# Kernel tuning notes

Hardware: AMD Instinct MI355X
Metric: run time of the kernel (lower is better)

Reference implementation:

```python
import jax, jax.numpy as jnp
import numpy as np

B, T, HIDDEN, QLR = 1, 2560, 7168, 1536
N_HEADS, HEAD_DIM, ROPE_DIM, TOPK = 64, 128, 64, 2048
LN_EPS = 1e-6


def _rope(x, cos, sin):
    # non-interleaved (half-split) rotary: pairs are (x[i], x[i+d/2])
    d = x.shape[-1] // 2
    x1, x2 = x[..., :d], x[..., d:]
    return jnp.concatenate([x1 * cos - x2 * sin, x1 * sin + x2 * cos], axis=-1)


def setup_inputs() -> dict:
    key = jax.random.key(0)
    ks = jax.random.split(key, 6)
    x = jax.random.normal(ks[0], (B, T, HIDDEN), dtype=jnp.float32)
    qr = jax.random.normal(ks[1], (B, T, QLR), dtype=jnp.float32)
    # rope tables (theta = 10000)
    inv_freq = 1.0 / (10000.0 ** (jnp.arange(0, ROPE_DIM, 2, dtype=jnp.float32) / ROPE_DIM))
    angles = jnp.arange(T, dtype=jnp.float32)[:, None] * inv_freq[None, :]  # [T, 32]
    freqs_cos = jnp.cos(angles)
    freqs_sin = jnp.sin(angles)
    # causal additive mask
    i = jnp.arange(T)
    mask = jnp.where(i[None, :, None] >= i[None, None, :], 0.0, -1e9).astype(jnp.float32)  # [1,T,T]
    # params (torch Linear stored transposed so y = x @ W)
    s = 0.02
    wq_b = jax.random.normal(ks[2], (QLR, N_HEADS * HEAD_DIM), dtype=jnp.float32) * s
    wk_w = jax.random.normal(ks[3], (HIDDEN, HEAD_DIM), dtype=jnp.float32) * s
    k_gamma = jnp.ones((HEAD_DIM,), dtype=jnp.float32)
    k_beta = jnp.zeros((HEAD_DIM,), dtype=jnp.float32)
    wproj = jax.random.normal(ks[4], (HIDDEN, N_HEADS), dtype=jnp.float32) * s
    return {"x": x, "qr": qr, "freqs_cos": freqs_cos, "freqs_sin": freqs_sin,
            "mask": mask, "wq_b": wq_b, "wk_w": wk_w, "k_gamma": k_gamma,
            "k_beta": k_beta, "wproj": wproj}


def reference(x, qr, freqs_cos, freqs_sin, mask, wq_b, wk_w, k_gamma, k_beta, wproj):
    bsz, seqlen, _ = x.shape
    # queries
    q = (qr @ wq_b).reshape(bsz, seqlen, N_HEADS, HEAD_DIM)
    q_pe, q_nope = q[..., :ROPE_DIM], q[..., ROPE_DIM:]
    q_pe = _rope(q_pe, freqs_cos[None, :, None, :], freqs_sin[None, :, None, :])
    q = jnp.concatenate([q_pe, q_nope], axis=-1)  # [B,T,H,D]
    # keys: layernorm(wk(x))
    k = x @ wk_w  # [B,T,D]
    mu = jnp.mean(k, axis=-1, keepdims=True)
    var = jnp.mean(jnp.square(k - mu), axis=-1, keepdims=True)
    k = (k - mu) / jnp.sqrt(var + LN_EPS) * k_gamma + k_beta
    k_pe, k_nope = k[..., :ROPE_DIM], k[..., ROPE_DIM:]
    k_pe = _rope(k_pe, freqs_cos[None, :, :], freqs_sin[None, :, :])
    k = jnp.concatenate([k_pe, k_nope], axis=-1)  # [B,S,D]
    # per-head weights
    weights = (x @ wproj) * (N_HEADS ** -0.5) * (HEAD_DIM ** -0.5)  # [B,T,H]
    # relu score + weighted head reduce
    logits = jax.nn.relu(jnp.einsum('bthd,bsd->btsh', q, k))  # [B,T,S,H]
    index_score = jnp.einsum('btsh,bth->bts', logits, weights) + mask
    # top-k + scatter mask
    kk = min(TOPK, seqlen)
    _, topk_idx = jax.lax.top_k(index_score, kk)  # [B,T,K]
    index_mask = jnp.full((bsz, seqlen, seqlen), -1e9, dtype=jnp.float32)
    bi = jnp.arange(bsz)[:, None, None]
    ti = jnp.arange(seqlen)[None, :, None]
    index_mask = index_mask.at[bi, ti, topk_idx].set(0.0)
    return index_mask
```

## Files before the change

### kernel.cpp

```cpp
#include <hip/hip_runtime.h>
#include <cstdint>

#define T_SEQ   2560
#define HID     7168
#define QLRD    1536
#define NHEAD   64
#define HDIM    128
#define TOPK    2048
#define T0SEL   2048
#define NSEL    512

#define QHOFF 0
#define QLOFF 2097152
#define KOFF  4194304
#define WOFF  4521984
#define KHOFF 4554752
#define KLOFF 4718592
#define SOFF  5242880

typedef _Float16 half8 __attribute__((ext_vector_type(8)));
typedef _Float16 half4v __attribute__((ext_vector_type(4)));
typedef float    floatx16 __attribute__((ext_vector_type(16)));

__device__ __forceinline__ void lds_barrier() {
    asm volatile("s_waitcnt lgkmcnt(0)" ::: "memory");
    __builtin_amdgcn_s_barrier();
}

__global__ __launch_bounds__(384) void kw_kernel(
        const float* __restrict__ x, const float* __restrict__ wk,
        const float* __restrict__ wp, float* __restrict__ Pk,
        float* __restrict__ Pw, long pkstride, long pwstride, int klen) {
    const int t0 = blockIdx.x * 64;
    const int chunk = blockIdx.y;
    const int k0 = chunk * klen;
    const int kl = min(klen, HID - k0);
    const int steps = kl >> 5;
    float* pk = Pk + (size_t)chunk * pkstride;
    float* pw = Pw + (size_t)chunk * pwstride;

    const int tid = threadIdx.x;
    const int lane = tid & 63;
    const int wv = tid >> 6;
    const int wt = wv / 3;
    const int wn2 = wv % 3;
    const int l31 = lane & 31;
    const int kb = (lane >> 5) * 8;

    __shared__ __align__(16) _Float16 Ah[64 * 40];
    __shared__ __align__(16) _Float16 Al[64 * 40];
    __shared__ __align__(16) _Float16 Bh[192 * 40];
    __shared__ __align__(16) _Float16 Bl[192 * 40];

    const int am = tid >> 2;
    const int ak = (tid & 3) * 8;
    const int bkr = (tid / 48) * 4;
    const int bnr = (tid % 48) * 4;

    const float* aptr = x + (size_t)(t0 + am) * HID + k0 + ak;
    const float* bsrc; int bld, bcol;
    if (bnr < 128) { bsrc = wk; bld = 128; bcol = bnr; }
    else           { bsrc = wp; bld = 64;  bcol = bnr - 128; }
    const float* bptr = bsrc + (size_t)(k0 + bkr) * bld + bcol;

    float4 pa0, pa1;
    if (tid < 256) { pa0 = *(const float4*)(aptr + 0); pa1 = *(const float4*)(aptr + 4); }
    float4 pb0 = *(const float4*)(bptr + 0 * (size_t)bld);
    float4 pb1 = *(const float4*)(bptr + 1 * (size_t)bld);
    float4 pb2 = *(const float4*)(bptr + 2 * (size_t)bld);
    float4 pb3 = *(const float4*)(bptr + 3 * (size_t)bld);

    floatx16 Z = {0.f,0.f,0.f,0.f,0.f,0.f,0.f,0.f,0.f,0.f,0.f,0.f,0.f,0.f,0.f,0.f};
    floatx16 Chh0 = Z, Chl0 = Z, Clh0 = Z;
    floatx16 Chh1 = Z, Chl1 = Z, Clh1 = Z;

    for (int ks = 0; ks < steps; ++ks) {
        lds_barrier();
        if (tid < 256) {
            float av[8];
            *(float4*)&av[0] = pa0; *(float4*)&av[4] = pa1;
            half8 ha, la;
#pragma unroll
            for (int i = 0; i < 8; ++i) {
                float v = av[i];
                _Float16 hi = (_Float16)v;
                ha[i] = hi;
                la[i] = (_Float16)(v - (float)hi);
            }
            *(half8*)&Ah[am * 40 + ak] = ha;
            *(half8*)&Al[am * 40 + ak] = la;
        }
        {
            float bv[4][4];
            *(float4*)&bv[0][0] = pb0; *(float4*)&bv[1][0] = pb1;
            *(float4*)&bv[2][0] = pb2; *(float4*)&bv[3][0] = pb3;
#pragma unroll
            for (int j = 0; j < 4; ++j) {
                half4v hb, lb;
#pragma unroll
                for (int i = 0; i < 4; ++i) {
                    float v = bv[i][j] * 64.0f;
                    _Float16 hi = (_Float16)v;
                    hb[i] = hi;
                    lb[i] = (_Float16)(v - (float)hi);
                }
                *(half4v*)&Bh[(bnr + j) * 40 + bkr] = hb;
                *(half4v*)&Bl[(bnr + j) * 40 + bkr] = lb;
            }
        }
        lds_barrier();
        if (ks + 1 < steps) {
            aptr += 32; bptr += (size_t)32 * bld;
            if (tid < 256) { pa0 = *(const float4*)(aptr + 0); pa1 = *(const float4*)(aptr + 4); }
            pb0 = *(const float4*)(bptr + 0 * (size_t)bld);
            pb1 = *(const float4*)(bptr + 1 * (size_t)bld);
            pb2 = *(const float4*)(bptr + 2 * (size_t)bld);
            pb3 = *(const float4*)(bptr + 3 * (size_t)bld);
        }
        __builtin_amdgcn_sched_barrier(0);
#pragma unroll
        for (int c = 0; c < 2; ++c) {
            const int ka = c * 16 + kb;
            half8 ah  = *(const half8*)&Ah[(wt * 32 + l31) * 40 + ka];
            half8 al  = *(const half8*)&Al[(wt * 32 + l31) * 40 + ka];
            half8 bh0 = *(const half8*)&Bh[(wn2 * 64 + l31) * 40 + ka];
            half8 bl0 = *(const half8*)&Bl[(wn2 * 64 + l31) * 40 + ka];
            half8 bh1 = *(const half8*)&Bh[(wn2 * 64 + 32 + l31) * 40 + ka];
            half8 bl1 = *(const half8*)&Bl[(wn2 * 64 + 32 + l31) * 40 + ka];
            Chh0 = __builtin_amdgcn_mfma_f32_32x32x16_f16(ah, bh0, Chh0, 0, 0, 0);
            Chl0 = __builtin_amdgcn_mfma_f32_32x32x16_f16(ah, bl0, Chl0, 0, 0, 0);
            Clh0 = __builtin_amdgcn_mfma_f32_32x32x16_f16(al, bh0, Clh0, 0, 0, 0);
            Chh1 = __builtin_amdgcn_mfma_f32_32x32x16_f16(ah, bh1, Chh1, 0, 0, 0);
            Chl1 = __builtin_amdgcn_mfma_f32_32x32x16_f16(ah, bl1, Chl1, 0, 0, 0);
            Clh1 = __builtin_amdgcn_mfma_f32_32x32x16_f16(al, bh1, Clh1, 0, 0, 0);
        }
    }

    const int rbase = wt * 32 + 4 * (lane >> 5);
#pragma unroll
    for (int r = 0; r < 16; ++r) {
        int trow = t0 + rbase + (r & 3) + 8 * (r >> 2);
        float v0 = ((Chh0[r] + Chl0[r]) + Clh0[r]) * 0.015625f;
        float v1 = ((Chh1[r] + Chl1[r]) + Clh1[r]) * 0.015625f;
        int c0 = wn2 * 64 + l31;
        if (wn2 < 2) {
            pk[(size_t)trow * 128 + c0] = v0;
            pk[(size_t)trow * 128 + c0 + 32] = v1;
        } else if (trow >= T0SEL) {
            pw[(size_t)(trow - T0SEL) * 64 + c0 - 128] = v0;
            pw[(size_t)(trow - T0SEL) * 64 + c0 - 96] = v1;
        }
    }
}

__global__ void reduce2_kernel(float* __restrict__ dk, const float* __restrict__ sk,
                               long kstr, float* __restrict__ dw,
                               const float* __restrict__ sw, long wstr, int nchunk) {
    int i = blockIdx.x * 256 + threadIdx.x;
    if (i < 327680) {
        float s = sk[i];
        for (int c = 1; c < nchunk; ++c) s += sk[(size_t)c * kstr + i];
        dk[i] = s;
    } else {
        int j = i - 327680;
        float s = sw[j];
        for (int c = 1; c < nchunk; ++c) s += sw[(size_t)c * wstr + j];
        dw[j] = s;
    }
}

__global__ void lnrope_kernel(const float* __restrict__ fcos, const float* __restrict__ fsin,
                              const float* __restrict__ gamma, const float* __restrict__ beta,
                              const float* __restrict__ Kbuf, float* __restrict__ Wbuf,
                              _Float16* __restrict__ KhG, _Float16* __restrict__ KlG) {
#pragma clang fp contract(off)
    const int s = blockIdx.x;
    const int d = threadIdx.x;
    __shared__ float red[128];
    __shared__ float kn[128];
    float kv = Kbuf[(size_t)s * 128 + d];
    red[d] = kv;
    __syncthreads();
    for (int off = 64; off > 0; off >>= 1) {
        if (d < off) red[d] += red[d + off];
        __syncthreads();
    }
    float mu = red[0] / 128.0f;
    __syncthreads();
    float dv = kv - mu;
    red[d] = dv * dv;
    __syncthreads();
    for (int off = 64; off > 0; off >>= 1) {
        if (d < off) red[d] += red[d + off];
        __syncthreads();
    }
    float var = red[0] / 128.0f;
    float nrm = dv / sqrtf(var + 1e-6f);
    nrm = nrm * gamma[d] + beta[d];
    kn[d] = nrm;
    __syncthreads();
    float o;
    if (d < 64) {
        int p = d & 31;
        float c = fcos[s * 32 + p], sn = fsin[s * 32 + p];
        if (d < 32) o = kn[d] * c - kn[d + 32] * sn;
        else        o = kn[d - 32] * sn + kn[d] * c;
    } else {
        o = kn[d];
    }
    _Float16 hi = (_Float16)o;
    _Float16 lo = (_Float16)(o - (float)hi);
    KhG[(size_t)s * 128 + d] = hi;
    KlG[(size_t)s * 128 + d] = lo;
    if (s >= T0SEL && d < 64) {
        Wbuf[(size_t)(s - T0SEL) * 64 + d] *= (0.125f * 0.08838834764831845f);
    }
}

__global__ __launch_bounds__(256, 2) void q_kernel(
        const float* __restrict__ qr, const float* __restrict__ wqb,
        const float* __restrict__ fcos, const float* __restrict__ fsin,
        _Float16* __restrict__ QhG, _Float16* __restrict__ QlG) {
    const int head = blockIdx.x;
    const int bx = blockIdx.y;
    const int tid = threadIdx.x;
    const int lane = tid & 63;
    const int wv = tid >> 6;
    const int wt = wv >> 1, wn = wv & 1;
    const int l31 = lane & 31;
    const int kb = (lane >> 5) * 8;

    __shared__ __align__(16) _Float16 Ah[64 * 40];
    __shared__ __align__(16) _Float16 Al[64 * 40];
    __shared__ __align__(16) _Float16 Bh[128 * 40];
    __shared__ __align__(16) _Float16 Bl[128 * 40];

    const int am = tid >> 2;
    const int ak = (tid & 3) * 8;
    const int bn = (tid & 31) * 4;
    const int bk = (tid >> 5) * 4;

    const float* aB = qr + (size_t)(T0SEL + bx * 64 + am) * QLRD + ak;
    const float* bB = wqb + (size_t)bk * 8192 + head * 128 + bn;

    float4 paA0, paA1, pbA0, pbA1, pbA2, pbA3;
    float4 paB0, paB1, pbB0, pbB1, pbB2, pbB3;

#define QLOADSET(PA0,PA1,PB0,PB1,PB2,PB3,KK) do {                              \
    const float* ap_ = aB + (size_t)(KK) * 32;                                 \
    const float* bp_ = bB + (size_t)(KK) * 32 * 8192;                          \
    PA0 = *(const float4*)(ap_ + 0);                                           \
    PA1 = *(const float4*)(ap_ + 4);                                           \
    PB0 = *(const float4*)(bp_ + 0 * 8192);                                    \
    PB1 = *(const float4*)(bp_ + 1 * 8192);                                    \
    PB2 = *(const float4*)(bp_ + 2 * 8192);                                    \
    PB3 = *(const float4*)(bp_ + 3 * 8192);                                    \
} while (0)

#define QCONVERT(PA0,PA1,PB0,PB1,PB2,PB3) do {                                 \
    float av[8];                                                               \
    *(float4*)&av[0] = PA0; *(float4*)&av[4] = PA1;                            \
    half8 ha, la;                                                              \
    _Pragma("unroll")                                                          \
    for (int i = 0; i < 8; ++i) {                                              \
        float v = av[i];                                                       \
        _Float16 hi = (_Float16)v;                                             \
        ha[i] = hi;                                                            \
        la[i] = (_Float16)(v - (float)hi);                                     \
    }                                                                          \
    *(half8*)&Ah[am * 40 + ak] = ha;                                           \
    *(half8*)&Al[am * 40 + ak] = la;                                           \
    float bv[4][4];                                                            \
    *(float4*)&bv[0][0] = PB0; *(float4*)&bv[1][0] = PB1;                      \
    *(float4*)&bv[2][0] = PB2; *(float4*)&bv[3][0] = PB3;                      \
    _Pragma("unroll")                                                          \
    for (int j = 0; j < 4; ++j) {                                              \
        half4v hb, lb;                                                         \
        _Pragma("unroll")                                                      \
        for (int i = 0; i < 4; ++i) {                                          \
            float v = bv[i][j] * 64.0f;                                        \
            _Float16 hi = (_Float16)v;                                         \
            hb[i] = hi;                                                        \
            lb[i] = (_Float16)(v - (float)hi);                                 \
        }                                                                      \
        *(half4v*)&Bh[(bn + j) * 40 + bk] = hb;                                \
        *(half4v*)&Bl[(bn + j) * 40 + bk] = lb;                                \
    }                                                                          \
} while (0)

#define QMFMA() do {                                                           \
    __builtin_amdgcn_s_setprio(1);                                             \
    _Pragma("unroll")                                                          \
    for (int c = 0; c < 2; ++c) {                                              \
        const int ka = c * 16 + kb;                                            \
        half8 ah = *(const half8*)&Ah[(wt * 32 + l31) * 40 + ka];              \
        half8 al = *(const half8*)&Al[(wt * 32 + l31) * 40 + ka];              \
        half8 bh0 = *(const half8*)&Bh[(wn * 64 + l31) * 40 + ka];             \
        half8 bl0 = *(const half8*)&Bl[(wn * 64 + l31) * 40 + ka];             \
        half8 bh1 = *(const half8*)&Bh[(wn * 64 + 32 + l31) * 40 + ka];        \
        half8 bl1 = *(const half8*)&Bl[(wn * 64 + 32 + l31) * 40 + ka];        \
        Chh0 = __builtin_amdgcn_mfma_f32_32x32x16_f16(ah, bh0, Chh0, 0, 0, 0); \
        Chl0 = __builtin_amdgcn_mfma_f32_32x32x16_f16(ah, bl0, Chl0, 0, 0, 0); \
        Clh0 = __builtin_amdgcn_mfma_f32_32x32x16_f16(al, bh0, Clh0, 0, 0, 0); \
        Chh1 = __builtin_amdgcn_mfma_f32_32x32x16_f16(ah, bh1, Chh1, 0, 0, 0); \
        Chl1 = __builtin_amdgcn_mfma_f32_32x32x16_f16(ah, bl1, Chl1, 0, 0, 0); \
        Clh1 = __builtin_amdgcn_mfma_f32_32x32x16_f16(al, bh1, Clh1, 0, 0, 0); \
    }                                                                          \
    __builtin_amdgcn_s_setprio(0);                                             \
} while (0)

    floatx16 Z = {0.f,0.f,0.f,0.f,0.f,0.f,0.f,0.f,0.f,0.f,0.f,0.f,0.f,0.f,0.f,0.f};
    floatx16 Chh0 = Z, Chl0 = Z, Clh0 = Z;
    floatx16 Chh1 = Z, Chl1 = Z, Clh1 = Z;

    const int steps = QLRD / 32;
    QLOADSET(paA0, paA1, pbA0, pbA1, pbA2, pbA3, 0);
    QLOADSET(paB0, paB1, pbB0, pbB1, pbB2, pbB3, 1);

    for (int ks = 0; ks < steps; ks += 2) {
        lds_barrier();
        QCONVERT(paA0, paA1, pbA0, pbA1, pbA2, pbA3);
        lds_barrier();
        QLOADSET(paA0, paA1, pbA0, pbA1, pbA2, pbA3, min(ks + 2, steps - 1));
        __builtin_amdgcn_sched_barrier(0);
        QMFMA();

        lds_barrier();
        QCONVERT(paB0, paB1, pbB0, pbB1, pbB2, pbB3);
        lds_barrier();
        QLOADSET(paB0, paB1, pbB0, pbB1, pbB2, pbB3, min(ks + 3, steps - 1));
        __builtin_amdgcn_sched_barrier(0);
        QMFMA();
    }
#undef QLOADSET
#undef QCONVERT
#undef QMFMA

    {
#pragma clang fp contract(off)
        const int tbase = bx * 64 + wt * 32 + 4 * (lane >> 5);
#pragma unroll
        for (int r = 0; r < 16; ++r) {
            int tl = tbase + (r & 3) + 8 * (r >> 2);
            float v0 = ((Chh0[r] + Chl0[r]) + Clh0[r]) * 0.015625f;
            float v1 = ((Chh1[r] + Chl1[r]) + Clh1[r]) * 0.015625f;
            float o0, o1;
            if (wn == 0) {
                int tg = T0SEL + tl;
                float c = fcos[tg * 32 + l31];
                float s = fsin[tg * 32 + l31];
                o0 = v0 * c - v1 * s;
                o1 = v0 * s + v1 * c;
            } else {
                o0 = v0; o1 = v1;
            }
            int d0 = wn * 64 + l31;
            size_t off = (size_t)head * 65536 + (size_t)tl * 128;
            _Float16 h0 = (_Float16)o0;
            _Float16 h1 = (_Float16)o1;
            QhG[off + d0] = h0;
            QlG[off + d0] = (_Float16)(o0 - (float)h0);
            QhG[off + d0 + 32] = h1;
            QlG[off + d0 + 32] = (_Float16)(o1 - (float)h1);
        }
    }
}

__global__ __launch_bounds__(256) void score_kernel(
        const _Float16* __restrict__ Qh, const _Float16* __restrict__ Ql,
        const _Float16* __restrict__ Kh, const _Float16* __restrict__ Kl,
        const float* __restrict__ Wbuf, float* __restrict__ S0,
        float* __restrict__ S1, int hcnt) {
    const int bid = blockIdx.x;
    const int tt0 = (bid & 15) * 32;
    const int s0  = (bid >> 4) * 128;
    const int hb  = blockIdx.y * hcnt;
    float* __restrict__ dst = blockIdx.y ? S1 : S0;
    const int tid = threadIdx.x;
    const int wv  = tid >> 6;
    const int lane = tid & 63;
    const int l31 = lane & 31;
    const int kb  = (lane >> 5) * 8;

    __shared__ __align__(16) _Float16 AhA[32 * 136];
    __shared__ __align__(16) _Float16 AlA[32 * 136];
    __shared__ __align__(16) _Float16 AhB[32 * 136];
    __shared__ __align__(16) _Float16 AlB[32 * 136];
    __shared__ float WsT[64 * 36];

    half8 Bh[8], Bl[8];
    {
        const int srow = s0 + wv * 32 + l31;
        const _Float16* kh = Kh + (size_t)srow * 128 + kb;
        const _Float16* kl = Kl + (size_t)srow * 128 + kb;
#pragma unroll
        for (int c = 0; c < 8; ++c) {
            Bh[c] = *(const half8*)(kh + c * 16);
            Bl[c] = *(const half8*)(kl + c * 16);
        }
    }
#pragma unroll
    for (int r = 0; r < 8; ++r) {
        int idx = tid + 256 * r;
        int row = idx >> 6, h = idx & 63;
        WsT[h * 36 + row] = Wbuf[(size_t)(tt0 + row) * 64 + h];
    }

    const int srow0 = tid >> 4;
    const int scc0  = (tid & 15) * 8;
    const int srow1 = srow0 + 16;
    const int scc1  = scc0;

    const _Float16* qhp = Qh + (size_t)hb * 65536 + (size_t)tt0 * 128;
    const _Float16* qlp = Ql + (size_t)hb * 65536 + (size_t)tt0 * 128;

    half8 sh0 = *(const half8*)&qhp[srow0 * 128 + scc0];
    half8 sh1 = *(const half8*)&qhp[srow1 * 128 + scc1];
    half8 sl0 = *(const half8*)&qlp[srow0 * 128 + scc0];
    half8 sl1 = *(const half8*)&qlp[srow1 * 128 + scc1];
    *(half8*)&AhA[srow0 * 136 + scc0] = sh0;
    *(half8*)&AhA[srow1 * 136 + scc1] = sh1;
    *(half8*)&AlA[srow0 * 136 + scc0] = sl0;
    *(half8*)&AlA[srow1 * 136 + scc1] = sl1;
    qhp += 65536; qlp += 65536;
    sh0 = *(const half8*)&qhp[srow0 * 128 + scc0];
    sh1 = *(const half8*)&qhp[srow1 * 128 + scc1];
    sl0 = *(const half8*)&qlp[srow0 * 128 + scc0];
    sl1 = *(const half8*)&qlp[srow1 * 128 + scc1];
    __builtin_amdgcn_sched_barrier(0);
    lds_barrier();

    float S[16];
#pragma unroll
    for (int r = 0; r < 16; ++r) S[r] = 0.0f;

#define SCORE_COMPUTE(AH, AL, HIDX)                                            \
    {                                                                          \
        floatx16 C0 = {0.f,0.f,0.f,0.f,0.f,0.f,0.f,0.f,                        \
                       0.f,0.f,0.f,0.f,0.f,0.f,0.f,0.f};                       \
        floatx16 C2 = C0, C3 = C0;                                             \
        __builtin_amdgcn_s_setprio(1);                                         \
        _Pragma("unroll")                                                      \
        for (int c = 0; c < 8; ++c) {                                          \
            half8 a_h = *(const half8*)&AH[l31 * 136 + c * 16 + kb];           \
            half8 a_l = *(const half8*)&AL[l31 * 136 + c * 16 + kb];           \
            C0 = __builtin_amdgcn_mfma_f32_32x32x16_f16(a_h, Bh[c], C0, 0, 0, 0); \
            C2 = __builtin_amdgcn_mfma_f32_32x32x16_f16(a_h, Bl[c], C2, 0, 0, 0); \
            C3 = __builtin_amdgcn_mfma_f32_32x32x16_f16(a_l, Bh[c], C3, 0, 0, 0); \
        }                                                                      \
        __builtin_amdgcn_s_setprio(0);                                         \
        const float* wb = &WsT[(HIDX) * 36 + 4 * (lane >> 5)];                 \
        float4 w0 = *(const float4*)(wb + 0);                                  \
        float4 w1 = *(const float4*)(wb + 8);                                  \
        float4 w2 = *(const float4*)(wb + 16);                                 \
        float4 w3 = *(const float4*)(wb + 24);                                 \
        float w[16] = {w0.x, w0.y, w0.z, w0.w, w1.x, w1.y, w1.z, w1.w,         \
                       w2.x, w2.y, w2.z, w2.w, w3.x, w3.y, w3.z, w3.w};        \
        _Pragma("unroll")                                                      \
        for (int r = 0; r < 16; ++r) {                                         \
            float L = (C0[r] + C2[r]) + C3[r];                                 \
            S[r] += w[r] * fmaxf(L, 0.0f);                                     \
        }                                                                      \
    }

    for (int h = 0; h < hcnt; h += 2) {
        SCORE_COMPUTE(AhA, AlA, hb + h)
        *(half8*)&AhB[srow0 * 136 + scc0] = sh0;
        *(half8*)&AhB[srow1 * 136 + scc1] = sh1;
        *(half8*)&AlB[srow0 * 136 + scc0] = sl0;
        *(half8*)&AlB[srow1 * 136 + scc1] = sl1;
        qhp += 65536; qlp += 65536;
        sh0 = *(const half8*)&qhp[srow0 * 128 + scc0];
        sh1 = *(const half8*)&qhp[srow1 * 128 + scc1];
        sl0 = *(const half8*)&qlp[srow0 * 128 + scc0];
        sl1 = *(const half8*)&qlp[srow1 * 128 + scc1];
        __builtin_amdgcn_sched_barrier(0);
        lds_barrier();

        SCORE_COMPUTE(AhB, AlB, hb + h + 1)
        *(half8*)&AhA[srow0 * 136 + scc0] = sh0;
        *(half8*)&AhA[srow1 * 136 + scc1] = sh1;
        *(half8*)&AlA[srow0 * 136 + scc0] = sl0;
        *(half8*)&AlA[srow1 * 136 + scc1] = sl1;
        qhp += 65536; qlp += 65536;
        sh0 = *(const half8*)&qhp[srow0 * 128 + scc0];
        sh1 = *(const half8*)&qhp[srow1 * 128 + scc1];
        sl0 = *(const half8*)&qlp[srow0 * 128 + scc0];
        sl1 = *(const half8*)&qlp[srow1 * 128 + scc1];
        __builtin_amdgcn_sched_barrier(0);
        lds_barrier();
    }
#undef SCORE_COMPUTE

    const int scol = s0 + wv * 32 + l31;
#pragma unroll
    for (int r = 0; r < 16; ++r) {
        int trow = tt0 + (r & 3) + 8 * (r >> 2) + 4 * (lane >> 5);
        dst[(size_t)trow * 2560 + scol] = S[r] + 0.0f;
    }
}

__global__ void finalize_kernel(float* __restrict__ out, const float* __restrict__ S1) {
    const int row_id = blockIdx.x;
    const int tid = threadIdx.x;

    if (row_id < T0SEL) {
        const float4 zero4 = make_float4(0.0f, 0.0f, 0.0f, 0.0f);
        const float4 neg4 = make_float4(-1000000000.0f, -1000000000.0f,
                                        -1000000000.0f, -1000000000.0f);
        for (int i = tid; i < T_SEQ / 4; i += 256) {
            *(float4*)&out[(size_t)row_id * T_SEQ + i * 4] = (i * 4 < TOPK) ? zero4 : neg4;
        }
        return;
    }

    const int t = row_id;
    const int n = t + 1;
    float* row = out + (size_t)t * T_SEQ;
    const float* s1p = S1 ? (S1 + (size_t)(t - T0SEL) * T_SEQ) : nullptr;

    __shared__ unsigned U[T_SEQ];
    __shared__ int hist[256];
    __shared__ int aux[256];
    __shared__ unsigned sh_prefix;
    __shared__ int sh_kneed;

    for (int i = tid; i < T_SEQ; i += 256) {
        unsigned u = 0u;
        if (i < n) {
            float sc = row[i];
            if (s1p) sc += s1p[i];
            int b = __float_as_int(sc);
            u = (b < 0) ? ~((unsigned)b) : (((unsigned)b) | 0x80000000u);
        }
        U[i] = u;
    }
    if (tid == 0) { sh_prefix = 0u; sh_kneed = TOPK; }
    __syncthreads();

    for (int pass = 0; pass < 4; ++pass) {
        const int shift = 24 - 8 * pass;
        const unsigned himask = (pass == 0) ? 0u : (0xFFFFFFFFu << (shift + 8));
        hist[tid] = 0;
        __syncthreads();
        const unsigned pre = sh_prefix;
        const int kneed = sh_kneed;
        for (int i = tid; i < T_SEQ; i += 256) {
            unsigned u = U[i];
            if ((u & himask) == pre) atomicAdd(&hist[(u >> shift) & 255], 1);
        }
        __syncthreads();
        aux[tid] = hist[tid];
        __syncthreads();
        for (int off = 1; off < 256; off <<= 1) {
            int a = (tid + off < 256) ? aux[tid + off] : 0;
            __syncthreads();
            aux[tid] += a;
            __syncthreads();
        }
        int above = (tid < 255) ? aux[tid + 1] : 0;
        if (above < kneed && kneed <= aux[tid]) {
            sh_prefix = pre | (((unsigned)tid) << shift);
            sh_kneed = kneed - above;
        }
        __syncthreads();
    }
    const unsigned theta = sh_prefix;
    const int r = sh_kneed;

    const int s_lo = tid * 10, s_hi = s_lo + 10;
    int c = 0;
    for (int s = s_lo; s < s_hi; ++s) c += (U[s] == theta);
    aux[tid] = c;
    __syncthreads();
    for (int off = 1; off < 256; off <<= 1) {
        int a = (tid >= off) ? aux[tid - off] : 0;
        __syncthreads();
        aux[tid] += a;
        __syncthreads();
    }
    int rank = aux[tid] - c;
    for (int s = s_lo; s < s_hi; ++s) {
        unsigned u = U[s];
        bool sel = (u > theta) || (u == theta && rank < r);
        if (u == theta) ++rank;
        row[s] = sel ? 0.0f : -1000000000.0f;
    }
}

extern "C" void kernel_launch(void* const* d_in, const int* in_sizes, int n_in,
                              void* d_out, int out_size, void* d_ws, size_t ws_size,
                              hipStream_t stream) {
    (void)in_sizes; (void)n_in; (void)out_size;
    const float* x     = (const float*)d_in[0];
    const float* qr    = (const float*)d_in[1];
    const float* fcos  = (const float*)d_in[2];
    const float* fsin  = (const float*)d_in[3];
    const float* wqb   = (const float*)d_in[5];
    const float* wk    = (const float*)d_in[6];
    const float* gamma = (const float*)d_in[7];
    const float* beta  = (const float*)d_in[8];
    const float* wp    = (const float*)d_in[9];

    float* out  = (float*)d_out;
    float* Kbuf = out + KOFF;
    float* Wbuf = out + WOFF;
    float* Sbuf = out + SOFF;
    _Float16* QhG = (_Float16*)(out + QHOFF);
    _Float16* QlG = (_Float16*)(out + QLOFF);
    _Float16* KhG = (_Float16*)(out + KHOFF);
    _Float16* KlG = (_Float16*)(out + KLOFF);

    const size_t need = (size_t)(6 * 327680 + 6 * 32768) * 4;
    int nchunk; int klen; float *Pk, *Pw; long pkstride, pwstride;
    if (ws_size >= need) {
        nchunk = 6; klen = 1216;
        Pk = (float*)d_ws;            pkstride = 327680;
        Pw = (float*)d_ws + 1966080;  pwstride = 32768;
    } else {
        nchunk = 2; klen = 3584;
        Pk = out + KOFF;  pkstride = 360448;
        Pw = out + WOFF;  pwstride = 360448;
    }

    const size_t s1_need = (size_t)NSEL * T_SEQ * sizeof(float);
    float* S1 = (ws_size >= s1_need) ? (float*)d_ws : nullptr;

    kw_kernel<<<dim3(40, nchunk), 384, 0, stream>>>(x, wk, wp, Pk, Pw, pkstride, pwstride, klen);
    reduce2_kernel<<<1408, 256, 0, stream>>>(Kbuf, Pk, pkstride, Wbuf, Pw, pwstride, nchunk);
    lnrope_kernel<<<T_SEQ, 128, 0, stream>>>(fcos, fsin, gamma, beta, Kbuf, Wbuf, KhG, KlG);
    q_kernel<<<dim3(64, 8), 256, 0, stream>>>(qr, wqb, fcos, fsin, QhG, QlG);
    if (S1) {
        score_kernel<<<dim3(320, 2), 256, 0, stream>>>(QhG, QlG, KhG, KlG, Wbuf, Sbuf, S1, 32);
    } else {
        score_kernel<<<dim3(320, 1), 256, 0, stream>>>(QhG, QlG, KhG, KlG, Wbuf, Sbuf, nullptr, 64);
    }
    finalize_kernel<<<T_SEQ, 256, 0, stream>>>(out, S1);
}
```

Baseline: 393.5 us.

## Double-buffer LDS tiles and XOR-swizzle layout in kw and q GEMM kernels

Both split-fp16 GEMM kernels (kw_kernel and q_kernel) get two LDS buffer sets. The MFMA work on one buffer now overlaps the fp32-to-fp16 conversion into the other, which cuts the two barriers per k-step down to one. An XOR swizzle on the k offset within each row is also applied to the LDS stores and reads to reduce bank conflicts. The cost is double the LDS footprint, which may lower occupancy, and q_kernel drops its second register prefetch set.

```diff
diff --git a/kernel.cpp b/kernel.cpp
--- a/kernel.cpp
+++ b/kernel.cpp
@@ -26,6 +26,8 @@
     asm volatile("s_waitcnt lgkmcnt(0)" ::: "memory");
     __builtin_amdgcn_s_barrier();
 }
+
+#define SWZ(row) ((((row) >> 3) & 3) << 3)
 
 __global__ __launch_bounds__(384) void kw_kernel(
         const float* __restrict__ x, const float* __restrict__ wk,
@@ -47,94 +49,125 @@
     const int l31 = lane & 31;
     const int kb = (lane >> 5) * 8;
 
-    __shared__ __align__(16) _Float16 Ah[64 * 40];
-    __shared__ __align__(16) _Float16 Al[64 * 40];
-    __shared__ __align__(16) _Float16 Bh[192 * 40];
-    __shared__ __align__(16) _Float16 Bl[192 * 40];
+    __shared__ __align__(16) _Float16 Ah0[64 * 40], Al0[64 * 40];
+    __shared__ __align__(16) _Float16 Bh0[192 * 40], Bl0[192 * 40];
+    __shared__ __align__(16) _Float16 Ah1[64 * 40], Al1[64 * 40];
+    __shared__ __align__(16) _Float16 Bh1[192 * 40], Bl1[192 * 40];
 
     const int am = tid >> 2;
     const int ak = (tid & 3) * 8;
+    const int akS = ak ^ SWZ(am);
     const int bkr = (tid / 48) * 4;
     const int bnr = (tid % 48) * 4;
 
-    const float* aptr = x + (size_t)(t0 + am) * HID + k0 + ak;
+    const float* aB = x + (size_t)(t0 + am) * HID + k0 + ak;
     const float* bsrc; int bld, bcol;
     if (bnr < 128) { bsrc = wk; bld = 128; bcol = bnr; }
     else           { bsrc = wp; bld = 64;  bcol = bnr - 128; }
-    const float* bptr = bsrc + (size_t)(k0 + bkr) * bld + bcol;
-
-    float4 pa0, pa1;
-    if (tid < 256) { pa0 = *(const float4*)(aptr + 0); pa1 = *(const float4*)(aptr + 4); }
-    float4 pb0 = *(const float4*)(bptr + 0 * (size_t)bld);
-    float4 pb1 = *(const float4*)(bptr + 1 * (size_t)bld);
-    float4 pb2 = *(const float4*)(bptr + 2 * (size_t)bld);
-    float4 pb3 = *(const float4*)(bptr + 3 * (size_t)bld);
+    const float* bB = bsrc + (size_t)(k0 + bkr) * bld + bcol;
+
+    float4 pa0, pa1, pb0, pb1, pb2, pb3;
+
+#define KWLOAD(KK) do {                                                        \
+    const float* ap_ = aB + (size_t)(KK) * 32;                                 \
+    const float* bp_ = bB + (size_t)(KK) * 32 * bld;                           \
+    if (tid < 256) { pa0 = *(const float4*)(ap_ + 0);                          \
+                     pa1 = *(const float4*)(ap_ + 4); }                        \
+    pb0 = *(const float4*)(bp_ + 0 * (size_t)bld);                             \
+    pb1 = *(const float4*)(bp_ + 1 * (size_t)bld);                             \
+    pb2 = *(const float4*)(bp_ + 2 * (size_t)bld);                             \
+    pb3 = *(const float4*)(bp_ + 3 * (size_t)bld);                             \
+} while (0)
+
+#define KWCONVERT(AH, AL, BH, BL) do {                                         \
+    if (tid < 256) {                                                           \
+        float av[8];                                                           \
+        *(float4*)&av[0] = pa0; *(float4*)&av[4] = pa1;                        \
+        half8 ha, la;                                                          \
+        _Pragma("unroll")                                                      \
+        for (int i = 0; i < 8; ++i) {                                          \
+            float v = av[i];                                                   \
+            _Float16 hi = (_Float16)v;                                         \
+            ha[i] = hi;                                                        \
+            la[i] = (_Float16)(v - (float)hi);                                 \
+        }                                                                      \
+        *(half8*)&AH[am * 40 + akS] = ha;                                      \
+        *(half8*)&AL[am * 40 + akS] = la;                                      \
+    }                                                                          \
+    {                                                                          \
+        float bv[4][4];                                                        \
+        *(float4*)&bv[0][0] = pb0; *(float4*)&bv[1][0] = pb1;                  \
+        *(float4*)&bv[2][0] = pb2; *(float4*)&bv[3][0] = pb3;                  \
+        _Pragma("unroll")                                                      \
+        for (int j = 0; j < 4; ++j) {                                          \
+            const int bkS = bkr ^ SWZ(bnr + j);                                \
+            half4v hb, lb;                                                     \
+            _Pragma("unroll")                                                  \
+            for (int i = 0; i < 4; ++i) {                                      \
+                float v = bv[i][j] * 64.0f;                                    \
+                _Float16 hi = (_Float16)v;                                     \
+                hb[i] = hi;                                                    \
+                lb[i] = (_Float16)(v - (float)hi);                             \
+            }                                                                  \
+            *(half4v*)&BH[(bnr + j) * 40 + bkS] = hb;                          \
+            *(half4v*)&BL[(bnr + j) * 40 + bkS] = lb;                          \
+        }                                                                      \
+    }                                                                          \
+} while (0)
+
+    const int rowA  = wt * 32 + l31;
+    const int xA    = SWZ(rowA);
+    const int rowB0 = wn2 * 64 + l31;
+    const int xB0   = SWZ(rowB0);
+    const int rowB1 = rowB0 + 32;
+    const int xB1   = SWZ(rowB1);
+
+#define KWMFMA(AH, AL, BH, BL) do {                                            \
+    __builtin_amdgcn_s_setprio(1);                                             \
+    _Pragma("unroll")                                                          \
+    for (int c = 0; c < 2; ++c) {                                              \
+        const int ka = c * 16 + kb;                                            \
+        half8 ah  = *(const half8*)&AH[rowA * 40 + (ka ^ xA)];                 \
+        half8 al  = *(const half8*)&AL[rowA * 40 + (ka ^ xA)];                 \
+        half8 bh0 = *(const half8*)&BH[rowB0 * 40 + (ka ^ xB0)];               \
+        half8 bl0 = *(const half8*)&BL[rowB0 * 40 + (ka ^ xB0)];               \
+        half8 bh1 = *(const half8*)&BH[rowB1 * 40 + (ka ^ xB1)];               \
+        half8 bl1 = *(const half8*)&BL[rowB1 * 40 + (ka ^ xB1)];               \
+        Chh0 = __builtin_amdgcn_mfma_f32_32x32x16_f16(ah, bh0, Chh0, 0, 0, 0); \
+        Chl0 = __builtin_amdgcn_mfma_f32_32x32x16_f16(ah, bl0, Chl0, 0, 0, 0); \
+        Clh0 = __builtin_amdgcn_mfma_f32_32x32x16_f16(al, bh0, Clh0, 0, 0, 0); \
+        Chh1 = __builtin_amdgcn_mfma_f32_32x32x16_f16(ah, bh1, Chh1, 0, 0, 0); \
+        Chl1 = __builtin_amdgcn_mfma_f32_32x32x16_f16(ah, bl1, Chl1, 0, 0, 0); \
+        Clh1 = __builtin_amdgcn_mfma_f32_32x32x16_f16(al, bh1, Clh1, 0, 0, 0); \
+    }                                                                          \
+    __builtin_amdgcn_s_setprio(0);                                             \
+} while (0)
 
     floatx16 Z = {0.f,0.f,0.f,0.f,0.f,0.f,0.f,0.f,0.f,0.f,0.f,0.f,0.f,0.f,0.f,0.f};
     floatx16 Chh0 = Z, Chl0 = Z, Clh0 = Z;
     floatx16 Chh1 = Z, Chl1 = Z, Clh1 = Z;
 
-    for (int ks = 0; ks < steps; ++ks) {
+    KWLOAD(0);
+    KWCONVERT(Ah0, Al0, Bh0, Bl0);
+    KWLOAD(1);
+    __builtin_amdgcn_sched_barrier(0);
+    lds_barrier();
+
+    for (int ks = 0; ks < steps; ks += 2) {
+        KWMFMA(Ah0, Al0, Bh0, Bl0);
+        KWCONVERT(Ah1, Al1, Bh1, Bl1);
+        KWLOAD(min(ks + 2, steps - 1));
+        __builtin_amdgcn_sched_barrier(0);
         lds_barrier();
-        if (tid < 256) {
-            float av[8];
-            *(float4*)&av[0] = pa0; *(float4*)&av[4] = pa1;
-            half8 ha, la;
-#pragma unroll
-            for (int i = 0; i < 8; ++i) {
-                float v = av[i];
-                _Float16 hi = (_Float16)v;
-                ha[i] = hi;
-                la[i] = (_Float16)(v - (float)hi);
-            }
-            *(half8*)&Ah[am * 40 + ak] = ha;
-            *(half8*)&Al[am * 40 + ak] = la;
-        }
-        {
-            float bv[4][4];
-            *(float4*)&bv[0][0] = pb0; *(float4*)&bv[1][0] = pb1;
-            *(float4*)&bv[2][0] = pb2; *(float4*)&bv[3][0] = pb3;
-#pragma unroll
-            for (int j = 0; j < 4; ++j) {
-                half4v hb, lb;
-#pragma unroll
-                for (int i = 0; i < 4; ++i) {
-                    float v = bv[i][j] * 64.0f;
-                    _Float16 hi = (_Float16)v;
-                    hb[i] = hi;
-                    lb[i] = (_Float16)(v - (float)hi);
-                }
-                *(half4v*)&Bh[(bnr + j) * 40 + bkr] = hb;
-                *(half4v*)&Bl[(bnr + j) * 40 + bkr] = lb;
-            }
-        }
+        KWMFMA(Ah1, Al1, Bh1, Bl1);
+        KWCONVERT(Ah0, Al0, Bh0, Bl0);
+        KWLOAD(min(ks + 3, steps - 1));
+        __builtin_amdgcn_sched_barrier(0);
         lds_barrier();
-        if (ks + 1 < steps) {
-            aptr += 32; bptr += (size_t)32 * bld;
-            if (tid < 256) { pa0 = *(const float4*)(aptr + 0); pa1 = *(const float4*)(aptr + 4); }
-            pb0 = *(const float4*)(bptr + 0 * (size_t)bld);
-            pb1 = *(const float4*)(bptr + 1 * (size_t)bld);
-            pb2 = *(const float4*)(bptr + 2 * (size_t)bld);
-            pb3 = *(const float4*)(bptr + 3 * (size_t)bld);
-        }
-        __builtin_amdgcn_sched_barrier(0);
-#pragma unroll
-        for (int c = 0; c < 2; ++c) {
-            const int ka = c * 16 + kb;
-            half8 ah  = *(const half8*)&Ah[(wt * 32 + l31) * 40 + ka];
-            half8 al  = *(const half8*)&Al[(wt * 32 + l31) * 40 + ka];
-            half8 bh0 = *(const half8*)&Bh[(wn2 * 64 + l31) * 40 + ka];
-            half8 bl0 = *(const half8*)&Bl[(wn2 * 64 + l31) * 40 + ka];
-            half8 bh1 = *(const half8*)&Bh[(wn2 * 64 + 32 + l31) * 40 + ka];
-            half8 bl1 = *(const half8*)&Bl[(wn2 * 64 + 32 + l31) * 40 + ka];
-            Chh0 = __builtin_amdgcn_mfma_f32_32x32x16_f16(ah, bh0, Chh0, 0, 0, 0);
-            Chl0 = __builtin_amdgcn_mfma_f32_32x32x16_f16(ah, bl0, Chl0, 0, 0, 0);
-            Clh0 = __builtin_amdgcn_mfma_f32_32x32x16_f16(al, bh0, Clh0, 0, 0, 0);
-            Chh1 = __builtin_amdgcn_mfma_f32_32x32x16_f16(ah, bh1, Chh1, 0, 0, 0);
-            Chl1 = __builtin_amdgcn_mfma_f32_32x32x16_f16(ah, bl1, Chl1, 0, 0, 0);
-            Clh1 = __builtin_amdgcn_mfma_f32_32x32x16_f16(al, bh1, Clh1, 0, 0, 0);
-        }
-    }
+    }
+#undef KWLOAD
+#undef KWCONVERT
+#undef KWMFMA
 
     const int rbase = wt * 32 + 4 * (lane >> 5);
 #pragma unroll
@@ -230,36 +263,36 @@
     const int l31 = lane & 31;
     const int kb = (lane >> 5) * 8;
 
-    __shared__ __align__(16) _Float16 Ah[64 * 40];
-    __shared__ __align__(16) _Float16 Al[64 * 40];
-    __shared__ __align__(16) _Float16 Bh[128 * 40];
-    __shared__ __align__(16) _Float16 Bl[128 * 40];
+    __shared__ __align__(16) _Float16 Ah0[64 * 40], Al0[64 * 40];
+    __shared__ __align__(16) _Float16 Bh0[128 * 40], Bl0[128 * 40];
+    __shared__ __align__(16) _Float16 Ah1[64 * 40], Al1[64 * 40];
+    __shared__ __align__(16) _Float16 Bh1[128 * 40], Bl1[128 * 40];
 
     const int am = tid >> 2;
     const int ak = (tid & 3) * 8;
+    const int akS = ak ^ SWZ(am);
     const int bn = (tid & 31) * 4;
     const int bk = (tid >> 5) * 4;
 
     const float* aB = qr + (size_t)(T0SEL + bx * 64 + am) * QLRD + ak;
     const float* bB = wqb + (size_t)bk * 8192 + head * 128 + bn;
 
-    float4 paA0, paA1, pbA0, pbA1, pbA2, pbA3;
-    float4 paB0, paB1, pbB0, pbB1, pbB2, pbB3;
-
-#define QLOADSET(PA0,PA1,PB0,PB1,PB2,PB3,KK) do {                              \
+    float4 pa0, pa1, pb0, pb1, pb2, pb3;
+
+#define QLOAD(KK) do {                                                         \
     const float* ap_ = aB + (size_t)(KK) * 32;                                 \
     const float* bp_ = bB + (size_t)(KK) * 32 * 8192;                          \
-    PA0 = *(const float4*)(ap_ + 0);                                           \
-    PA1 = *(const float4*)(ap_ + 4);                                           \
-    PB0 = *(const float4*)(bp_ + 0 * 8192);                                    \
-    PB1 = *(const float4*)(bp_ + 1 * 8192);                                    \
-    PB2 = *(const float4*)(bp_ + 2 * 8192);                                    \
-    PB3 = *(const float4*)(bp_ + 3 * 8192);                                    \
+    pa0 = *(const float4*)(ap_ + 0);                                           \
+    pa1 = *(const float4*)(ap_ + 4);                                           \
+    pb0 = *(const float4*)(bp_ + 0 * 8192);                                    \
+    pb1 = *(const float4*)(bp_ + 1 * 8192);                                    \
+    pb2 = *(const float4*)(bp_ + 2 * 8192);                                    \
+    pb3 = *(const float4*)(bp_ + 3 * 8192);                                    \
 } while (0)
 
-#define QCONVERT(PA0,PA1,PB0,PB1,PB2,PB3) do {                                 \
+#define QCONVERT(AH, AL, BH, BL) do {                                          \
     float av[8];                                                               \
-    *(float4*)&av[0] = PA0; *(float4*)&av[4] = PA1;                            \
+    *(float4*)&av[0] = pa0; *(float4*)&av[4] = pa1;                            \
     half8 ha, la;                                                              \
     _Pragma("unroll")                                                          \
     for (int i = 0; i < 8; ++i) {                                              \
@@ -268,13 +301,14 @@
         ha[i] = hi;                                                            \
         la[i] = (_Float16)(v - (float)hi);                                     \
     }                                                                          \
-    *(half8*)&Ah[am * 40 + ak] = ha;                                           \
-    *(half8*)&Al[am * 40 + ak] = la;                                           \
+    *(half8*)&AH[am * 40 + akS] = ha;                                          \
+    *(half8*)&AL[am * 40 + akS] = la;                                          \
     float bv[4][4];                                                            \
-    *(float4*)&bv[0][0] = PB0; *(float4*)&bv[1][0] = PB1;                      \
-    *(float4*)&bv[2][0] = PB2; *(float4*)&bv[3][0] = PB3;                      \
+    *(float4*)&bv[0][0] = pb0; *(float4*)&bv[1][0] = pb1;                      \
+    *(float4*)&bv[2][0] = pb2; *(float4*)&bv[3][0] = pb3;                      \
     _Pragma("unroll")                                                          \
     for (int j = 0; j < 4; ++j) {                                              \
+        const int bkS = bk ^ SWZ(bn + j);                                      \
         half4v hb, lb;                                                         \
         _Pragma("unroll")                                                      \
         for (int i = 0; i < 4; ++i) {                                          \
@@ -283,22 +317,29 @@
             hb[i] = hi;                                                        \
             lb[i] = (_Float16)(v - (float)hi);                                 \
         }                                                                      \
-        *(half4v*)&Bh[(bn + j) * 40 + bk] = hb;                                \
-        *(half4v*)&Bl[(bn + j) * 40 + bk] = lb;                                \
+        *(half4v*)&BH[(bn + j) * 40 + bkS] = hb;                               \
+        *(half4v*)&BL[(bn + j) * 40 + bkS] = lb;                               \
     }                                                                          \
 } while (0)
 
-#define QMFMA() do {                                                           \
+    const int rowA  = wt * 32 + l31;
+    const int xA    = SWZ(rowA);
+    const int rowB0 = wn * 64 + l31;
+    const int xB0   = SWZ(rowB0);
+    const int rowB1 = rowB0 + 32;
+    const int xB1   = SWZ(rowB1);
+
+#define QMFMA(AH, AL, BH, BL) do {                                             \
     __builtin_amdgcn_s_setprio(1);                                             \
     _Pragma("unroll")                                                          \
     for (int c = 0; c < 2; ++c) {                                              \
         const int ka = c * 16 + kb;                                            \
-        half8 ah = *(const half8*)&Ah[(wt * 32 + l31) * 40 + ka];              \
-        half8 al = *(const half8*)&Al[(wt * 32 + l31) * 40 + ka];              \
-        half8 bh0 = *(const half8*)&Bh[(wn * 64 + l31) * 40 + ka];             \
-        half8 bl0 = *(const half8*)&Bl[(wn * 64 + l31) * 40 + ka];             \
-        half8 bh1 = *(const half8*)&Bh[(wn * 64 + 32 + l31) * 40 + ka];        \
-        half8 bl1 = *(const half8*)&Bl[(wn * 64 + 32 + l31) * 40 + ka];        \
+        half8 ah  = *(const half8*)&AH[rowA * 40 + (ka ^ xA)];                 \
+        half8 al  = *(const half8*)&AL[rowA * 40 + (ka ^ xA)];                 \
+        half8 bh0 = *(const half8*)&BH[rowB0 * 40 + (ka ^ xB0)];               \
+        half8 bl0 = *(const half8*)&BL[rowB0 * 40 + (ka ^ xB0)];               \
+        half8 bh1 = *(const half8*)&BH[rowB1 * 40 + (ka ^ xB1)];               \
+        half8 bl1 = *(const half8*)&BL[rowB1 * 40 + (ka ^ xB1)];               \
         Chh0 = __builtin_amdgcn_mfma_f32_32x32x16_f16(ah, bh0, Chh0, 0, 0, 0); \
         Chl0 = __builtin_amdgcn_mfma_f32_32x32x16_f16(ah, bl0, Chl0, 0, 0, 0); \
         Clh0 = __builtin_amdgcn_mfma_f32_32x32x16_f16(al, bh0, Clh0, 0, 0, 0); \
@@ -314,25 +355,26 @@
     floatx16 Chh1 = Z, Chl1 = Z, Clh1 = Z;
 
     const int steps = QLRD / 32;
-    QLOADSET(paA0, paA1, pbA0, pbA1, pbA2, pbA3, 0);
-    QLOADSET(paB0, paB1, pbB0, pbB1, pbB2, pbB3, 1);
+
+    QLOAD(0);
+    QCONVERT(Ah0, Al0, Bh0, Bl0);
+    QLOAD(1);
+    __builtin_amdgcn_sched_barrier(0);
+    lds_barrier();
 
     for (int ks = 0; ks < steps; ks += 2) {
+        QMFMA(Ah0, Al0, Bh0, Bl0);
+        QCONVERT(Ah1, Al1, Bh1, Bl1);
+        QLOAD(min(ks + 2, steps - 1));
+        __builtin_amdgcn_sched_barrier(0);
         lds_barrier();
-        QCONVERT(paA0, paA1, pbA0, pbA1, pbA2, pbA3);
+        QMFMA(Ah1, Al1, Bh1, Bl1);
+        QCONVERT(Ah0, Al0, Bh0, Bl0);
+        QLOAD(min(ks + 3, steps - 1));
+        __builtin_amdgcn_sched_barrier(0);
         lds_barrier();
-        QLOADSET(paA0, paA1, pbA0, pbA1, pbA2, pbA3, min(ks + 2, steps - 1));
-        __builtin_amdgcn_sched_barrier(0);
-        QMFMA();
-
-        lds_barrier();
-        QCONVERT(paB0, paB1, pbB0, pbB1, pbB2, pbB3);
-        lds_barrier();
-        QLOADSET(paB0, paB1, pbB0, pbB1, pbB2, pbB3, min(ks + 3, steps - 1));
-        __builtin_amdgcn_sched_barrier(0);
-        QMFMA();
-    }
-#undef QLOADSET
+    }
+#undef QLOAD
 #undef QCONVERT
 #undef QMFMA
 
```

After: 362.7 us. 1.08x faster.
